# Kernel optimization log

Measured on AMD Instinct MI355X. Metric: run time of the kernel, lower is better.

Reference implementation:

```python
import jax, jax.numpy as jnp
import numpy as np

D, K, HID, NBLK, N = 128, 256, 256, 2, 4096

def setup_inputs() -> dict:
    key = jax.random.key(0)
    ks = jax.random.split(key, 12)
    inp = {
        'x': jax.random.normal(ks[0], (N, D), jnp.float32),
        'x_hat': jax.random.normal(ks[1], (N, D), jnp.float32),
        'base_codebook': jax.random.normal(ks[2], (K, D), jnp.float32) * 0.1,
        # concat_proj: Linear(2D -> D), torch weight layout (out, in)
        'Wp': jax.random.normal(ks[3], (D, 2 * D), jnp.float32) / np.sqrt(2 * D),
        'bp': jnp.zeros((D,), jnp.float32),
        # residual blocks stacked over NBLK: Linear(D->HID), ReLU, Linear(HID->D)
        'W1': jax.random.normal(ks[4], (NBLK, HID, D), jnp.float32) / np.sqrt(D),
        'b1': jnp.zeros((NBLK, HID), jnp.float32),
        'W2': jax.random.normal(ks[5], (NBLK, D, HID), jnp.float32) / np.sqrt(HID),
        'b2': jnp.zeros((NBLK, D), jnp.float32),
    }
    return inp

def _forward(x, x_hat, base_codebook, Wp, bp, W1, b1, W2, b2):
    # concat_proj([x_hat, cbar]) decomposed: avoids materializing (N,K,2D)
    x_part = x_hat @ Wp[:, :D].T                      # (N, D)
    c_part = base_codebook @ Wp[:, D:].T + bp          # (K, D)
    C = x_part[:, None, :] + c_part[None, :, :]        # (N, K, D)
    for i in range(NBLK):
        h = jax.nn.relu(jnp.einsum('nkd,hd->nkh', C, W1[i]) + b1[i])
        C = C + jnp.einsum('nkh,dh->nkd', h, W2[i]) + b2[i]
    r = x - x_hat                                      # (N, D)
    dists = jnp.sum((r[:, None, :] - C) ** 2, axis=-1) # (N, K)
    codes = jnp.argmin(dists, axis=-1)                 # (N,)
    c_sel = jnp.take_along_axis(C, codes[:, None, None], axis=1)[:, 0, :]
    x_hat_new = x_hat + c_sel
    return codes, x_hat_new, r, c_sel

def reference(x, x_hat, base_codebook, Wp, bp, W1, b1, W2, b2):
    return _forward(x, x_hat, base_codebook, Wp, bp, W1, b1, W2, b2)
```

## Files before the change

kernel.cpp:

```cpp
#include <hip/hip_runtime.h>


#define QD    128
#define QK    256
#define QHID  256
#define QNBLK 2
#define QN    4096

typedef _Float16 f16;
typedef _Float16 f16x8  __attribute__((ext_vector_type(8)));
typedef float    f32x16 __attribute__((ext_vector_type(16)));
typedef unsigned u32x2  __attribute__((ext_vector_type(2)));

#define WS_CPART 0
#define WS_W1H   131072
#define WS_W1L   262144
#define WS_W2H   393216
#define WS_W2L   524288
#define WS_PART  655360

#define L_WBUF  0
#define L_B1    65536
#define L_B2    67584
#define L_REDD  68608
#define L_REDI  69120
#define L_XP    69632
#define L_XH    70144
#define L_RS    70656
#define L_TOTAL 71168

static __device__ __forceinline__ f32x16 MF32(f16x8 a, f16x8 b, f32x16 c) {
    return __builtin_amdgcn_mfma_f32_32x32x16_f16(a, b, c, 0, 0, 0);
}
static __device__ __forceinline__ unsigned pkrtz(float a, float b) {
    return __builtin_bit_cast(unsigned, __builtin_amdgcn_cvt_pkrtz(a, b));
}
static __device__ __forceinline__ float f32lo(unsigned p) {
    return (float)__builtin_bit_cast(f16, (unsigned short)(p & 0xffffu));
}
static __device__ __forceinline__ float f32hi(unsigned p) {
    return (float)__builtin_bit_cast(f16, (unsigned short)(p >> 16));
}
static __device__ __forceinline__ u32x2 plswap(unsigned a, unsigned b) {
    return __builtin_amdgcn_permlane32_swap(a, b, false, false);
}
static __device__ __forceinline__ void gload_lds16(const void* g, void* l) {
    __builtin_amdgcn_global_load_lds(
        (const __attribute__((address_space(1))) unsigned*)g,
        (__attribute__((address_space(3))) unsigned*)l, 16, 0, 0);
}

template<int RB>
static __device__ __forceinline__ void split_frags(f32x16 a, f16x8& fh, f16x8& fl) {
    unsigned P0 = pkrtz(a[RB + 0], a[RB + 1]);
    unsigned P1 = pkrtz(a[RB + 2], a[RB + 3]);
    unsigned Q0 = pkrtz(a[RB + 4], a[RB + 5]);
    unsigned Q1 = pkrtz(a[RB + 6], a[RB + 7]);
    unsigned L0 = pkrtz(a[RB + 0] - f32lo(P0), a[RB + 1] - f32hi(P0));
    unsigned L1 = pkrtz(a[RB + 2] - f32lo(P1), a[RB + 3] - f32hi(P1));
    unsigned L2 = pkrtz(a[RB + 4] - f32lo(Q0), a[RB + 5] - f32hi(Q0));
    unsigned L3 = pkrtz(a[RB + 6] - f32lo(Q1), a[RB + 7] - f32hi(Q1));
    u32x2 s0 = plswap(P0, Q0);
    u32x2 s1 = plswap(P1, Q1);
    u32x2 t0 = plswap(L0, L2);
    u32x2 t1 = plswap(L1, L3);
    uint4 hw = make_uint4(s0.x, s1.x, s0.y, s1.y);
    uint4 lw = make_uint4(t0.x, t1.x, t0.y, t1.y);
    fh = __builtin_bit_cast(f16x8, hw);
    fl = __builtin_bit_cast(f16x8, lw);
}

__global__ __launch_bounds__(128) void qinco_prep(
    const float* __restrict__ cb, const float* __restrict__ Wp,
    const float* __restrict__ bp, const float* __restrict__ W1,
    const float* __restrict__ W2, char* __restrict__ ws) {
    const int blk = blockIdx.x;
    const int t = threadIdx.x;
    __shared__ float row[QD];

    if (blk < 256) {
        float* cpart = (float*)(ws + WS_CPART);
        row[t] = cb[blk * QD + t];
        __syncthreads();
        float acc = bp[t];
        const float* wr = Wp + (size_t)t * (2 * QD) + QD;
        #pragma unroll 8
        for (int e = 0; e < QD; ++e) acc = fmaf(row[e], wr[e], acc);
        cpart[blk * QD + t] = acc;
    } else if (blk < 384) {
        if (t < 64) {
            const int cid = blk - 256;
            const int b = cid >> 6, hc = (cid >> 3) & 7, kc = cid & 7;
            const int m = t & 31, g = t >> 5;
            f16* w1h = (f16*)(ws + WS_W1H);
            f16* w1l = (f16*)(ws + WS_W1L);
            #pragma unroll
            for (int j = 0; j < 8; ++j) {
                float wv = W1[((size_t)b * QHID + hc * 32 + m) * QD + kc * 16 + g * 8 + j];
                f16 hi = (f16)wv;
                size_t idx = ((size_t)cid * 64 + t) * 8 + j;
                w1h[idx] = hi;
                w1l[idx] = (f16)(wv - (float)hi);
            }
        }
    } else {
        if (t < 64) {
            const int e = blk - 384;
            const int b = e >> 6, hc = (e >> 3) & 7, dt = (e >> 1) & 3, kch = e & 1;
            const int m = t & 31, g = t >> 5;
            f16* w2h = (f16*)(ws + WS_W2H);
            f16* w2l = (f16*)(ws + WS_W2L);
            #pragma unroll
            for (int j = 0; j < 8; ++j) {
                float wv = W2[((size_t)b * QD + dt * 32 + m) * QHID + hc * 32 + kch * 16 + g * 8 + j];
                f16 hi = (f16)wv;
                size_t idx = ((size_t)e * 64 + t) * 8 + j;
                w2h[idx] = hi;
                w2l[idx] = (f16)(wv - (float)hi);
            }
        }
    }
}

__global__ __launch_bounds__(256, 2) void qinco_main(
    const float* __restrict__ x, const float* __restrict__ xh,
    const float* __restrict__ Wp,
    const float* __restrict__ b1g, const float* __restrict__ b2g,
    char* __restrict__ ws, float* __restrict__ out) {

    extern __shared__ char smem[];
    const int n = blockIdx.x >> 1;
    const int half = blockIdx.x & 1;
    const int t = threadIdx.x;
    const int w = t >> 6;
    const int l = t & 63;
    const int c32 = l & 31;
    const int g = l >> 5;
    const int baserow = w * 32;

    float* b1_s  = (float*)(smem + L_B1);
    float* b2_s  = (float*)(smem + L_B2);
    float* red_d = (float*)(smem + L_REDD);
    int*   red_i = (int*)(smem + L_REDI);
    float* xp_s  = (float*)(smem + L_XP);
    float* xh_s  = (float*)(smem + L_XH);
    float* r_s   = (float*)(smem + L_RS);

    const float* cpart = (const float*)(ws + WS_CPART);

    b1_s[t] = b1g[t];
    b1_s[t + 256] = b1g[t + 256];
    if (t < 2 * QD) b2_s[t] = b2g[t];
    if (t < QD) {
        float xv  = x[(size_t)n * QD + t];
        float xhv = xh[(size_t)n * QD + t];
        xh_s[t] = xhv;
        r_s[t]  = xv - xhv;
    }
    __syncthreads();

    if (t < QD) {
        const float4* wr = (const float4*)(Wp + (size_t)t * (2 * QD));
        const float4* xv = (const float4*)xh_s;
        float acc = 0.f;
        #pragma unroll
        for (int j = 0; j < QD / 4; ++j) {
            float4 a = wr[j], bv = xv[j];
            acc = fmaf(a.x, bv.x, acc);
            acc = fmaf(a.y, bv.y, acc);
            acc = fmaf(a.z, bv.z, acc);
            acc = fmaf(a.w, bv.w, acc);
        }
        xp_s[t] = acc;
    }
    __syncthreads();

    f32x16 Cacc[4];
    {
        const float* cprow = cpart + (size_t)(half * 128 + baserow + c32) * QD;
        #pragma unroll
        for (int dt = 0; dt < 4; ++dt)
            #pragma unroll
            for (int rq = 0; rq < 4; ++rq) {
                const int off = dt * 32 + 8 * rq + 4 * g;
                float4 cp  = *(const float4*)(cprow + off);
                float4 xp4 = *(const float4*)(xp_s + off);
                Cacc[dt][rq * 4 + 0] = cp.x + xp4.x;
                Cacc[dt][rq * 4 + 1] = cp.y + xp4.y;
                Cacc[dt][rq * 4 + 2] = cp.z + xp4.z;
                Cacc[dt][rq * 4 + 3] = cp.w + xp4.w;
            }
    }

    {
        const char* s0 = ws + (size_t)(w + 1) * 131072 + (size_t)l * 16;
        char* d0 = smem + L_WBUF + (size_t)w * 8192;
        #pragma unroll
        for (int ii = 0; ii < 8; ++ii)
            gload_lds16(s0 + (size_t)ii * 1024, d0 + (size_t)ii * 1024);
    }

    f16x8 cfh[8], cfl[8];

    #pragma unroll 1
    for (int iter = 0; iter < 16; ++iter) {
        asm volatile("s_waitcnt vmcnt(0)" ::: "memory");
        __builtin_amdgcn_s_barrier();
        asm volatile("" ::: "memory");

        if (iter < 15) {
            const int tt = iter + 1, bb = tt >> 3, hh = tt & 7;
            const char* s0 = ws + (size_t)(w + 1) * 131072 + (size_t)bb * 65536
                           + (size_t)hh * 8192 + (size_t)l * 16;
            char* d0 = smem + L_WBUF + (size_t)(tt & 1) * 32768 + (size_t)w * 8192;
            #pragma unroll
            for (int ii = 0; ii < 8; ++ii)
                gload_lds16(s0 + (size_t)ii * 1024, d0 + (size_t)ii * 1024);
        }

        const int b = iter >> 3;
        const int hc = iter & 7;

        if (hc == 0) {
            #pragma unroll
            for (int dt = 0; dt < 4; ++dt) {
                split_frags<0>(Cacc[dt], cfh[dt * 2 + 0], cfl[dt * 2 + 0]);
                split_frags<8>(Cacc[dt], cfh[dt * 2 + 1], cfl[dt * 2 + 1]);
            }
        }

        const char* wb = (const char*)smem + L_WBUF + (size_t)(iter & 1) * 32768
                       + (size_t)l * 16;

        f32x16 Ha;
        #pragma unroll
        for (int rq = 0; rq < 4; ++rq) {
            float4 bv = *(const float4*)(b1_s + b * QHID + hc * 32 + 8 * rq + 4 * g);
            Ha[rq * 4 + 0] = bv.x;
            Ha[rq * 4 + 1] = bv.y;
            Ha[rq * 4 + 2] = bv.z;
            Ha[rq * 4 + 3] = bv.w;
        }
        f16x8 wh = *(const f16x8*)(wb);
        f16x8 wl = *(const f16x8*)(wb + 8192);
        __builtin_amdgcn_s_setprio(1);
        #pragma unroll
        for (int kc = 0; kc < 8; ++kc) {
            f16x8 nh, nl;
            if (kc < 7) {
                nh = *(const f16x8*)(wb + (kc + 1) * 1024);
                nl = *(const f16x8*)(wb + 8192 + (kc + 1) * 1024);
            }
            Ha = MF32(wh, cfh[kc], Ha);
            Ha = MF32(wl, cfh[kc], Ha);
            Ha = MF32(wh, cfl[kc], Ha);
            if (kc < 7) { wh = nh; wl = nl; }
        }
        __builtin_amdgcn_s_setprio(0);

        #pragma unroll
        for (int r = 0; r < 16; ++r) Ha[r] = fmaxf(Ha[r], 0.f);

        f16x8 hfh0, hfl0, hfh1, hfl1;
        split_frags<0>(Ha, hfh0, hfl0);

        const char* q2h = wb + 16384;
        const char* q2l = wb + 24576;

        __builtin_amdgcn_s_setprio(1);
        #pragma unroll
        for (int dt = 0; dt < 4; ++dt) {
            f16x8 w2h0 = *(const f16x8*)(q2h + (size_t)(dt * 2) * 1024);
            f16x8 w2l0 = *(const f16x8*)(q2l + (size_t)(dt * 2) * 1024);
            Cacc[dt] = MF32(w2h0, hfh0, Cacc[dt]);
            Cacc[dt] = MF32(w2l0, hfh0, Cacc[dt]);
            Cacc[dt] = MF32(w2h0, hfl0, Cacc[dt]);
        }
        __builtin_amdgcn_s_setprio(0);

        split_frags<8>(Ha, hfh1, hfl1);

        __builtin_amdgcn_s_setprio(1);
        #pragma unroll
        for (int dt = 0; dt < 4; ++dt) {
            f16x8 w2h1 = *(const f16x8*)(q2h + (size_t)(dt * 2 + 1) * 1024);
            f16x8 w2l1 = *(const f16x8*)(q2l + (size_t)(dt * 2 + 1) * 1024);
            Cacc[dt] = MF32(w2h1, hfh1, Cacc[dt]);
            Cacc[dt] = MF32(w2l1, hfh1, Cacc[dt]);
            Cacc[dt] = MF32(w2h1, hfl1, Cacc[dt]);
        }
        __builtin_amdgcn_s_setprio(0);

        if (hc == 7) {
            #pragma unroll
            for (int dt = 0; dt < 4; ++dt)
                #pragma unroll
                for (int rq = 0; rq < 4; ++rq) {
                    float4 bv = *(const float4*)(b2_s + b * QD + dt * 32 + 8 * rq + 4 * g);
                    Cacc[dt][rq * 4 + 0] += bv.x;
                    Cacc[dt][rq * 4 + 1] += bv.y;
                    Cacc[dt][rq * 4 + 2] += bv.z;
                    Cacc[dt][rq * 4 + 3] += bv.w;
                }
        }
    }

    float pa = 0.f, pb = 0.f, pc = 0.f, pdm = 0.f;
    #pragma unroll
    for (int dt = 0; dt < 4; ++dt)
        #pragma unroll
        for (int rq = 0; rq < 4; ++rq) {
            float4 rr = *(const float4*)(r_s + dt * 32 + 8 * rq + 4 * g);
            float t0 = rr.x - Cacc[dt][rq * 4 + 0];
            float t1 = rr.y - Cacc[dt][rq * 4 + 1];
            float t2 = rr.z - Cacc[dt][rq * 4 + 2];
            float t3 = rr.w - Cacc[dt][rq * 4 + 3];
            pa = fmaf(t0, t0, pa);
            pb = fmaf(t1, t1, pb);
            pc = fmaf(t2, t2, pc);
            pdm = fmaf(t3, t3, pdm);
        }
    float pd = (pa + pb) + (pc + pdm);
    pd += __shfl_xor(pd, 32);
    if (l < 32) {
        red_d[baserow + l] = pd;
        red_i[baserow + l] = baserow + l;
    }
    __syncthreads();

    for (int off = 64; off > 0; off >>= 1) {
        if (t < off) {
            float d2 = red_d[t + off]; int i2 = red_i[t + off];
            float d1 = red_d[t];       int i1 = red_i[t];
            if (d2 < d1 || (d2 == d1 && i2 < i1)) { red_d[t] = d2; red_i[t] = i2; }
        }
        __syncthreads();
    }
    const int lcode = red_i[0];

    float* creg = out + (half == 0 ? (QN + 2 * (size_t)QN * QD) : (size_t)QN)
                + (size_t)n * QD;
    if (w == (lcode >> 5) && c32 == (lcode & 31)) {
        #pragma unroll
        for (int dt = 0; dt < 4; ++dt)
            #pragma unroll
            for (int rq = 0; rq < 4; ++rq)
                *(float4*)(creg + dt * 32 + 8 * rq + 4 * g) =
                    make_float4(Cacc[dt][rq * 4 + 0], Cacc[dt][rq * 4 + 1],
                                Cacc[dt][rq * 4 + 2], Cacc[dt][rq * 4 + 3]);
    }
    if (t == 0) {
        float2* pp = (float2*)(ws + WS_PART);
        pp[n * 2 + half] = make_float2(red_d[0], (float)(half * 128 + lcode));
    }
}

__global__ __launch_bounds__(128) void qinco_fin(
    const float* __restrict__ x, const float* __restrict__ xh,
    const char* __restrict__ ws, float* __restrict__ out) {
    const int n = blockIdx.x;
    const int t = threadIdx.x;
    const float2* pp = (const float2*)(ws + WS_PART);
    float2 p0 = pp[n * 2 + 0];
    float2 p1 = pp[n * 2 + 1];
    const int h = (p1.x < p0.x) ? 1 : 0;
    const float codef = h ? p1.y : p0.y;

    const size_t o_xh = QN + (size_t)n * QD;
    const size_t o_r  = QN + (size_t)QN * QD + (size_t)n * QD;
    const size_t o_cs = QN + 2 * (size_t)QN * QD + (size_t)n * QD;

    float c0 = out[o_cs + t];
    float c1 = out[o_xh + t];
    float cs = h ? c1 : c0;
    float xhv = xh[(size_t)n * QD + t];
    float xv  = x[(size_t)n * QD + t];

    if (t == 0) out[n] = codef;
    out[o_xh + t] = xhv + cs;
    out[o_r + t]  = xv - xhv;
    out[o_cs + t] = cs;
}

extern "C" void kernel_launch(void* const* d_in, const int* in_sizes, int n_in,
                              void* d_out, int out_size, void* d_ws, size_t ws_size,
                              hipStream_t stream) {
    const float* x   = (const float*)d_in[0];
    const float* xh  = (const float*)d_in[1];
    const float* cb  = (const float*)d_in[2];
    const float* Wp  = (const float*)d_in[3];
    const float* bp  = (const float*)d_in[4];
    const float* W1  = (const float*)d_in[5];
    const float* b1  = (const float*)d_in[6];
    const float* W2  = (const float*)d_in[7];
    const float* b2  = (const float*)d_in[8];
    float* out = (float*)d_out;

    qinco_prep<<<512, 128, 0, stream>>>(cb, Wp, bp, W1, W2, (char*)d_ws);

    (void)hipFuncSetAttribute((const void*)qinco_main,
                              hipFuncAttributeMaxDynamicSharedMemorySize, L_TOTAL);
    qinco_main<<<2 * QN, 256, L_TOTAL, stream>>>(x, xh, Wp, b1, b2,
                                                 (char*)d_ws, out);
    qinco_fin<<<QN, 128, 0, stream>>>(x, xh, (const char*)d_ws, out);
}
```

Measured before the change: 713.9 us.

## Split weight staging into W1/W2 phases to halve LDS and raise occupancy

Replaces the double-buffered 64KB weight staging with single 16KB buffers for W1 and W2, each loaded by two waves per plane. W2 tiles are fetched while the W1 MFMAs run, and the next W1 tile is fetched after a second barrier, during the W2 phase. This halves LDS use so launch bounds can request 4 blocks per CU instead of 2, trading an extra barrier per iteration and shorter prefetch distance for higher occupancy. Register pressure at 4 blocks per CU may force spills given the large accumulator arrays.

```diff
diff --git a/kernel.cpp b/kernel.cpp
--- a/kernel.cpp
+++ b/kernel.cpp
@@ -14,20 +14,18 @@
 
 #define WS_CPART 0
 #define WS_W1H   131072
-#define WS_W1L   262144
 #define WS_W2H   393216
-#define WS_W2L   524288
 #define WS_PART  655360
 
 #define L_WBUF  0
-#define L_B1    65536
-#define L_B2    67584
-#define L_REDD  68608
-#define L_REDI  69120
-#define L_XP    69632
-#define L_XH    70144
-#define L_RS    70656
-#define L_TOTAL 71168
+#define L_B1    32768
+#define L_B2    34816
+#define L_REDD  35840
+#define L_REDI  36352
+#define L_XP    36864
+#define L_XH    37376
+#define L_RS    37888
+#define L_TOTAL 38400
 
 static __device__ __forceinline__ f32x16 MF32(f16x8 a, f16x8 b, f32x16 c) {
     return __builtin_amdgcn_mfma_f32_32x32x16_f16(a, b, c, 0, 0, 0);
@@ -93,7 +91,7 @@
             const int b = cid >> 6, hc = (cid >> 3) & 7, kc = cid & 7;
             const int m = t & 31, g = t >> 5;
             f16* w1h = (f16*)(ws + WS_W1H);
-            f16* w1l = (f16*)(ws + WS_W1L);
+            f16* w1l = (f16*)(ws + WS_W1H + 131072);
             #pragma unroll
             for (int j = 0; j < 8; ++j) {
                 float wv = W1[((size_t)b * QHID + hc * 32 + m) * QD + kc * 16 + g * 8 + j];
@@ -109,7 +107,7 @@
             const int b = e >> 6, hc = (e >> 3) & 7, dt = (e >> 1) & 3, kch = e & 1;
             const int m = t & 31, g = t >> 5;
             f16* w2h = (f16*)(ws + WS_W2H);
-            f16* w2l = (f16*)(ws + WS_W2L);
+            f16* w2l = (f16*)(ws + WS_W2H + 131072);
             #pragma unroll
             for (int j = 0; j < 8; ++j) {
                 float wv = W2[((size_t)b * QD + dt * 32 + m) * QHID + hc * 32 + kch * 16 + g * 8 + j];
@@ -122,7 +120,7 @@
     }
 }
 
-__global__ __launch_bounds__(256, 2) void qinco_main(
+__global__ __launch_bounds__(256, 4) void qinco_main(
     const float* __restrict__ x, const float* __restrict__ xh,
     const float* __restrict__ Wp,
     const float* __restrict__ b1g, const float* __restrict__ b2g,
@@ -137,6 +135,8 @@
     const int c32 = l & 31;
     const int g = l >> 5;
     const int baserow = w * 32;
+    const int plane = w >> 1;
+    const int hfw = w & 1;
 
     float* b1_s  = (float*)(smem + L_B1);
     float* b2_s  = (float*)(smem + L_B2);
@@ -192,34 +192,36 @@
             }
     }
 
+    const size_t stg_off = (size_t)plane * 131072 + (size_t)hfw * 4096 + (size_t)l * 16;
+    char* const dstA = smem + L_WBUF + (size_t)plane * 8192 + (size_t)hfw * 4096;
+    char* const dstB = dstA + 16384;
+
+    asm volatile("s_waitcnt vmcnt(0)" ::: "memory");
     {
-        const char* s0 = ws + (size_t)(w + 1) * 131072 + (size_t)l * 16;
-        char* d0 = smem + L_WBUF + (size_t)w * 8192;
-        #pragma unroll
-        for (int ii = 0; ii < 8; ++ii)
-            gload_lds16(s0 + (size_t)ii * 1024, d0 + (size_t)ii * 1024);
+        const char* s0 = ws + WS_W1H + stg_off;
+        #pragma unroll
+        for (int ii = 0; ii < 4; ++ii)
+            gload_lds16(s0 + (size_t)ii * 1024, dstA + (size_t)ii * 1024);
     }
 
     f16x8 cfh[8], cfl[8];
 
     #pragma unroll 1
     for (int iter = 0; iter < 16; ++iter) {
+        const int b = iter >> 3;
+        const int hc = iter & 7;
+
         asm volatile("s_waitcnt vmcnt(0)" ::: "memory");
         __builtin_amdgcn_s_barrier();
         asm volatile("" ::: "memory");
 
-        if (iter < 15) {
-            const int tt = iter + 1, bb = tt >> 3, hh = tt & 7;
-            const char* s0 = ws + (size_t)(w + 1) * 131072 + (size_t)bb * 65536
-                           + (size_t)hh * 8192 + (size_t)l * 16;
-            char* d0 = smem + L_WBUF + (size_t)(tt & 1) * 32768 + (size_t)w * 8192;
-            #pragma unroll
-            for (int ii = 0; ii < 8; ++ii)
-                gload_lds16(s0 + (size_t)ii * 1024, d0 + (size_t)ii * 1024);
-        }
-
-        const int b = iter >> 3;
-        const int hc = iter & 7;
+        {
+            const char* s0 = ws + WS_W2H + (size_t)b * 65536 + (size_t)hc * 8192
+                           + stg_off;
+            #pragma unroll
+            for (int ii = 0; ii < 4; ++ii)
+                gload_lds16(s0 + (size_t)ii * 1024, dstB + (size_t)ii * 1024);
+        }
 
         if (hc == 0) {
             #pragma unroll
@@ -229,8 +231,7 @@
             }
         }
 
-        const char* wb = (const char*)smem + L_WBUF + (size_t)(iter & 1) * 32768
-                       + (size_t)l * 16;
+        const char* wb1 = (const char*)smem + L_WBUF + (size_t)l * 16;
 
         f32x16 Ha;
         #pragma unroll
@@ -241,15 +242,15 @@
             Ha[rq * 4 + 2] = bv.z;
             Ha[rq * 4 + 3] = bv.w;
         }
-        f16x8 wh = *(const f16x8*)(wb);
-        f16x8 wl = *(const f16x8*)(wb + 8192);
+        f16x8 wh = *(const f16x8*)(wb1);
+        f16x8 wl = *(const f16x8*)(wb1 + 8192);
         __builtin_amdgcn_s_setprio(1);
         #pragma unroll
         for (int kc = 0; kc < 8; ++kc) {
             f16x8 nh, nl;
             if (kc < 7) {
-                nh = *(const f16x8*)(wb + (kc + 1) * 1024);
-                nl = *(const f16x8*)(wb + 8192 + (kc + 1) * 1024);
+                nh = *(const f16x8*)(wb1 + (kc + 1) * 1024);
+                nl = *(const f16x8*)(wb1 + 8192 + (kc + 1) * 1024);
             }
             Ha = MF32(wh, cfh[kc], Ha);
             Ha = MF32(wl, cfh[kc], Ha);
@@ -260,18 +261,29 @@
 
         #pragma unroll
         for (int r = 0; r < 16; ++r) Ha[r] = fmaxf(Ha[r], 0.f);
-
         f16x8 hfh0, hfl0, hfh1, hfl1;
         split_frags<0>(Ha, hfh0, hfl0);
 
-        const char* q2h = wb + 16384;
-        const char* q2l = wb + 24576;
+        asm volatile("s_waitcnt vmcnt(0)" ::: "memory");
+        __builtin_amdgcn_s_barrier();
+        asm volatile("" ::: "memory");
+
+        if (iter < 15) {
+            const int t2 = iter + 1, bb = t2 >> 3, hh = t2 & 7;
+            const char* s0 = ws + WS_W1H + (size_t)bb * 65536 + (size_t)hh * 8192
+                           + stg_off;
+            #pragma unroll
+            for (int ii = 0; ii < 4; ++ii)
+                gload_lds16(s0 + (size_t)ii * 1024, dstA + (size_t)ii * 1024);
+        }
+
+        const char* wb2 = (const char*)smem + L_WBUF + 16384 + (size_t)l * 16;
 
         __builtin_amdgcn_s_setprio(1);
         #pragma unroll
         for (int dt = 0; dt < 4; ++dt) {
-            f16x8 w2h0 = *(const f16x8*)(q2h + (size_t)(dt * 2) * 1024);
-            f16x8 w2l0 = *(const f16x8*)(q2l + (size_t)(dt * 2) * 1024);
+            f16x8 w2h0 = *(const f16x8*)(wb2 + (size_t)(dt * 2) * 1024);
+            f16x8 w2l0 = *(const f16x8*)(wb2 + 8192 + (size_t)(dt * 2) * 1024);
             Cacc[dt] = MF32(w2h0, hfh0, Cacc[dt]);
             Cacc[dt] = MF32(w2l0, hfh0, Cacc[dt]);
             Cacc[dt] = MF32(w2h0, hfl0, Cacc[dt]);
@@ -283,8 +295,8 @@
         __builtin_amdgcn_s_setprio(1);
         #pragma unroll
         for (int dt = 0; dt < 4; ++dt) {
-            f16x8 w2h1 = *(const f16x8*)(q2h + (size_t)(dt * 2 + 1) * 1024);
-            f16x8 w2l1 = *(const f16x8*)(q2l + (size_t)(dt * 2 + 1) * 1024);
+            f16x8 w2h1 = *(const f16x8*)(wb2 + (size_t)(dt * 2 + 1) * 1024);
+            f16x8 w2l1 = *(const f16x8*)(wb2 + 8192 + (size_t)(dt * 2 + 1) * 1024);
             Cacc[dt] = MF32(w2h1, hfh1, Cacc[dt]);
             Cacc[dt] = MF32(w2l1, hfh1, Cacc[dt]);
             Cacc[dt] = MF32(w2h1, hfl1, Cacc[dt]);
```

After: 2.041 ms. 2.86x slower.

## Software-pipeline GEMM2 of previous hidden chunk with GEMM1 of current chunk

Applied to the files above, without the earlier changes.

Splits the shared weight staging into separate W1 and W2 double buffers and skews the loop so each iteration runs GEMM1 for hidden chunk i interleaved with GEMM2 for chunk i-1. Extra drain steps at the block boundary and after the loop finish the last GEMM2 and add b2. The goal is to break the serial dependency between the ReLU/split of H and the second MFMA chain, so independent MFMAs can overlap. In exchange it holds more live fragment registers, which may increase register pressure at 2 waves per SIMD.

```diff
diff --git a/kernel.cpp b/kernel.cpp
--- a/kernel.cpp
+++ b/kernel.cpp
@@ -14,12 +14,11 @@
 
 #define WS_CPART 0
 #define WS_W1H   131072
-#define WS_W1L   262144
 #define WS_W2H   393216
-#define WS_W2L   524288
 #define WS_PART  655360
 
-#define L_WBUF  0
+#define L_W1B   0
+#define L_W2B   32768
 #define L_B1    65536
 #define L_B2    67584
 #define L_REDD  68608
@@ -93,7 +92,7 @@
             const int b = cid >> 6, hc = (cid >> 3) & 7, kc = cid & 7;
             const int m = t & 31, g = t >> 5;
             f16* w1h = (f16*)(ws + WS_W1H);
-            f16* w1l = (f16*)(ws + WS_W1L);
+            f16* w1l = (f16*)(ws + WS_W1H + 131072);
             #pragma unroll
             for (int j = 0; j < 8; ++j) {
                 float wv = W1[((size_t)b * QHID + hc * 32 + m) * QD + kc * 16 + g * 8 + j];
@@ -109,7 +108,7 @@
             const int b = e >> 6, hc = (e >> 3) & 7, dt = (e >> 1) & 3, kch = e & 1;
             const int m = t & 31, g = t >> 5;
             f16* w2h = (f16*)(ws + WS_W2H);
-            f16* w2l = (f16*)(ws + WS_W2L);
+            f16* w2l = (f16*)(ws + WS_W2H + 131072);
             #pragma unroll
             for (int j = 0; j < 8; ++j) {
                 float wv = W2[((size_t)b * QD + dt * 32 + m) * QHID + hc * 32 + kch * 16 + g * 8 + j];
@@ -148,6 +147,10 @@
 
     const float* cpart = (const float*)(ws + WS_CPART);
 
+    const size_t stg = (size_t)(w >> 1) * 131072 + (size_t)(w & 1) * 4096
+                     + (size_t)l * 16;
+    const size_t dq  = (size_t)(w >> 1) * 8192 + (size_t)(w & 1) * 4096;
+
     b1_s[t] = b1g[t];
     b1_s[t + 256] = b1g[t + 256];
     if (t < 2 * QD) b2_s[t] = b2g[t];
@@ -157,6 +160,13 @@
         xh_s[t] = xhv;
         r_s[t]  = xv - xhv;
     }
+    {
+        const char* s0 = ws + WS_W1H + stg;
+        char* d0 = smem + L_W1B + dq;
+        #pragma unroll
+        for (int ii = 0; ii < 4; ++ii)
+            gload_lds16(s0 + (size_t)ii * 1024, d0 + (size_t)ii * 1024);
+    }
     __syncthreads();
 
     if (t < QD) {
@@ -192,36 +202,68 @@
             }
     }
 
-    {
-        const char* s0 = ws + (size_t)(w + 1) * 131072 + (size_t)l * 16;
-        char* d0 = smem + L_WBUF + (size_t)w * 8192;
-        #pragma unroll
-        for (int ii = 0; ii < 8; ++ii)
-            gload_lds16(s0 + (size_t)ii * 1024, d0 + (size_t)ii * 1024);
-    }
-
     f16x8 cfh[8], cfl[8];
+    f16x8 hfh0p, hfl0p, hfh1p, hfl1p;
+
+    #define GEMM2_DRAIN(wb2p, bb) {                                            \
+        __builtin_amdgcn_s_setprio(1);                                         \
+        _Pragma("unroll") for (int s = 0; s < 8; ++s) {                        \
+            f16x8 w2h = *(const f16x8*)((wb2p) + (size_t)s * 1024);            \
+            f16x8 w2l = *(const f16x8*)((wb2p) + 8192 + (size_t)s * 1024);     \
+            if ((s & 1) == 0) {                                                \
+                Cacc[s >> 1] = MF32(w2h, hfh0p, Cacc[s >> 1]);                 \
+                Cacc[s >> 1] = MF32(w2l, hfh0p, Cacc[s >> 1]);                 \
+                Cacc[s >> 1] = MF32(w2h, hfl0p, Cacc[s >> 1]);                 \
+            } else {                                                           \
+                Cacc[s >> 1] = MF32(w2h, hfh1p, Cacc[s >> 1]);                 \
+                Cacc[s >> 1] = MF32(w2l, hfh1p, Cacc[s >> 1]);                 \
+                Cacc[s >> 1] = MF32(w2h, hfl1p, Cacc[s >> 1]);                 \
+            }                                                                  \
+        }                                                                      \
+        __builtin_amdgcn_s_setprio(0);                                         \
+        _Pragma("unroll") for (int dt = 0; dt < 4; ++dt)                       \
+        _Pragma("unroll") for (int rq = 0; rq < 4; ++rq) {                     \
+            float4 bv = *(const float4*)(b2_s + (bb) * QD + dt * 32            \
+                                         + 8 * rq + 4 * g);                    \
+            Cacc[dt][rq * 4 + 0] += bv.x;                                      \
+            Cacc[dt][rq * 4 + 1] += bv.y;                                      \
+            Cacc[dt][rq * 4 + 2] += bv.z;                                      \
+            Cacc[dt][rq * 4 + 3] += bv.w;                                      \
+        } }
 
     #pragma unroll 1
     for (int iter = 0; iter < 16; ++iter) {
+        const int b = iter >> 3;
+        const int hc = iter & 7;
+
         asm volatile("s_waitcnt vmcnt(0)" ::: "memory");
         __builtin_amdgcn_s_barrier();
         asm volatile("" ::: "memory");
 
         if (iter < 15) {
-            const int tt = iter + 1, bb = tt >> 3, hh = tt & 7;
-            const char* s0 = ws + (size_t)(w + 1) * 131072 + (size_t)bb * 65536
-                           + (size_t)hh * 8192 + (size_t)l * 16;
-            char* d0 = smem + L_WBUF + (size_t)(tt & 1) * 32768 + (size_t)w * 8192;
-            #pragma unroll
-            for (int ii = 0; ii < 8; ++ii)
+            const int t2 = iter + 1;
+            const char* s0 = ws + WS_W1H + (size_t)(t2 >> 3) * 65536
+                           + (size_t)(t2 & 7) * 8192 + stg;
+            char* d0 = smem + L_W1B + (size_t)(t2 & 1) * 16384 + dq;
+            #pragma unroll
+            for (int ii = 0; ii < 4; ++ii)
                 gload_lds16(s0 + (size_t)ii * 1024, d0 + (size_t)ii * 1024);
         }
-
-        const int b = iter >> 3;
-        const int hc = iter & 7;
+        {
+            const char* s0 = ws + WS_W2H + (size_t)b * 65536
+                           + (size_t)hc * 8192 + stg;
+            char* d0 = smem + L_W2B + (size_t)(iter & 1) * 16384 + dq;
+            #pragma unroll
+            for (int ii = 0; ii < 4; ++ii)
+                gload_lds16(s0 + (size_t)ii * 1024, d0 + (size_t)ii * 1024);
+        }
+
+        const char* wb2p = (const char*)smem + L_W2B
+                         + (size_t)((iter + 1) & 1) * 16384 + (size_t)l * 16;
 
         if (hc == 0) {
+            if (iter == 8)
+                GEMM2_DRAIN(wb2p, 0)
             #pragma unroll
             for (int dt = 0; dt < 4; ++dt) {
                 split_frags<0>(Cacc[dt], cfh[dt * 2 + 0], cfl[dt * 2 + 0]);
@@ -229,9 +271,8 @@
             }
         }
 
-        const char* wb = (const char*)smem + L_WBUF + (size_t)(iter & 1) * 32768
-                       + (size_t)l * 16;
-
+        const char* wb1 = (const char*)smem + L_W1B
+                        + (size_t)(iter & 1) * 16384 + (size_t)l * 16;
         f32x16 Ha;
         #pragma unroll
         for (int rq = 0; rq < 4; ++rq) {
@@ -241,69 +282,56 @@
             Ha[rq * 4 + 2] = bv.z;
             Ha[rq * 4 + 3] = bv.w;
         }
-        f16x8 wh = *(const f16x8*)(wb);
-        f16x8 wl = *(const f16x8*)(wb + 8192);
+
         __builtin_amdgcn_s_setprio(1);
-        #pragma unroll
-        for (int kc = 0; kc < 8; ++kc) {
-            f16x8 nh, nl;
-            if (kc < 7) {
-                nh = *(const f16x8*)(wb + (kc + 1) * 1024);
-                nl = *(const f16x8*)(wb + 8192 + (kc + 1) * 1024);
-            }
-            Ha = MF32(wh, cfh[kc], Ha);
-            Ha = MF32(wl, cfh[kc], Ha);
-            Ha = MF32(wh, cfl[kc], Ha);
-            if (kc < 7) { wh = nh; wl = nl; }
+        if (hc != 0) {
+            #pragma unroll
+            for (int p = 0; p < 8; ++p) {
+                const int kc = p;
+                const int s = ((p & 3) << 1) | (p >> 2);
+                f16x8 wh  = *(const f16x8*)(wb1 + (size_t)kc * 1024);
+                f16x8 wl  = *(const f16x8*)(wb1 + 8192 + (size_t)kc * 1024);
+                f16x8 w2h = *(const f16x8*)(wb2p + (size_t)s * 1024);
+                f16x8 w2l = *(const f16x8*)(wb2p + 8192 + (size_t)s * 1024);
+                Ha = MF32(wh, cfh[kc], Ha);
+                Ha = MF32(wl, cfh[kc], Ha);
+                Ha = MF32(wh, cfl[kc], Ha);
+                if (p < 4) {
+                    Cacc[p & 3] = MF32(w2h, hfh0p, Cacc[p & 3]);
+                    Cacc[p & 3] = MF32(w2l, hfh0p, Cacc[p & 3]);
+                    Cacc[p & 3] = MF32(w2h, hfl0p, Cacc[p & 3]);
+                } else {
+                    Cacc[p & 3] = MF32(w2h, hfh1p, Cacc[p & 3]);
+                    Cacc[p & 3] = MF32(w2l, hfh1p, Cacc[p & 3]);
+                    Cacc[p & 3] = MF32(w2h, hfl1p, Cacc[p & 3]);
+                }
+            }
+        } else {
+            #pragma unroll
+            for (int kc = 0; kc < 8; ++kc) {
+                f16x8 wh = *(const f16x8*)(wb1 + (size_t)kc * 1024);
+                f16x8 wl = *(const f16x8*)(wb1 + 8192 + (size_t)kc * 1024);
+                Ha = MF32(wh, cfh[kc], Ha);
+                Ha = MF32(wl, cfh[kc], Ha);
+                Ha = MF32(wh, cfl[kc], Ha);
+            }
         }
         __builtin_amdgcn_s_setprio(0);
 
         #pragma unroll
         for (int r = 0; r < 16; ++r) Ha[r] = fmaxf(Ha[r], 0.f);
-
-        f16x8 hfh0, hfl0, hfh1, hfl1;
-        split_frags<0>(Ha, hfh0, hfl0);
-
-        const char* q2h = wb + 16384;
-        const char* q2l = wb + 24576;
-
-        __builtin_amdgcn_s_setprio(1);
-        #pragma unroll
-        for (int dt = 0; dt < 4; ++dt) {
-            f16x8 w2h0 = *(const f16x8*)(q2h + (size_t)(dt * 2) * 1024);
-            f16x8 w2l0 = *(const f16x8*)(q2l + (size_t)(dt * 2) * 1024);
-            Cacc[dt] = MF32(w2h0, hfh0, Cacc[dt]);
-            Cacc[dt] = MF32(w2l0, hfh0, Cacc[dt]);
-            Cacc[dt] = MF32(w2h0, hfl0, Cacc[dt]);
-        }
-        __builtin_amdgcn_s_setprio(0);
-
-        split_frags<8>(Ha, hfh1, hfl1);
-
-        __builtin_amdgcn_s_setprio(1);
-        #pragma unroll
-        for (int dt = 0; dt < 4; ++dt) {
-            f16x8 w2h1 = *(const f16x8*)(q2h + (size_t)(dt * 2 + 1) * 1024);
-            f16x8 w2l1 = *(const f16x8*)(q2l + (size_t)(dt * 2 + 1) * 1024);
-            Cacc[dt] = MF32(w2h1, hfh1, Cacc[dt]);
-            Cacc[dt] = MF32(w2l1, hfh1, Cacc[dt]);
-            Cacc[dt] = MF32(w2h1, hfl1, Cacc[dt]);
-        }
-        __builtin_amdgcn_s_setprio(0);
-
-        if (hc == 7) {
-            #pragma unroll
-            for (int dt = 0; dt < 4; ++dt)
-                #pragma unroll
-                for (int rq = 0; rq < 4; ++rq) {
-                    float4 bv = *(const float4*)(b2_s + b * QD + dt * 32 + 8 * rq + 4 * g);
-                    Cacc[dt][rq * 4 + 0] += bv.x;
-                    Cacc[dt][rq * 4 + 1] += bv.y;
-                    Cacc[dt][rq * 4 + 2] += bv.z;
-                    Cacc[dt][rq * 4 + 3] += bv.w;
-                }
-        }
-    }
+        split_frags<0>(Ha, hfh0p, hfl0p);
+        split_frags<8>(Ha, hfh1p, hfl1p);
+    }
+
+    asm volatile("s_waitcnt vmcnt(0)" ::: "memory");
+    __builtin_amdgcn_s_barrier();
+    asm volatile("" ::: "memory");
+    {
+        const char* wb2p = (const char*)smem + L_W2B + 16384 + (size_t)l * 16;
+        GEMM2_DRAIN(wb2p, 1)
+    }
+    #undef GEMM2_DRAIN
 
     float pa = 0.f, pb = 0.f, pc = 0.f, pdm = 0.f;
     #pragma unroll
```

Result: slower. 749.7 us (+5.0%).
